# Performance work log

Hardware: AMD Instinct MI355X
Metric: run time of the kernel (lower is better)

Reference implementation:

```python
import jax, jax.numpy as jnp
import numpy as np

N = 50000      # nodes
E = 500000     # edges
IN_FEAT = 128
OUT_FEAT = 128
R = 200        # num_relations
NB = 16        # num_bases -> 8x8 blocks
SI = IN_FEAT // NB   # submat_in = 8
SO = OUT_FEAT // NB  # submat_out = 8


def setup_inputs() -> dict:
    key = jax.random.key(0)
    k1, k2, k3, k4, k5, k6, k7 = jax.random.split(key, 7)
    h = jax.random.normal(k1, (N, IN_FEAT), dtype=jnp.float32)
    norm = jax.random.uniform(k2, (N, 1), dtype=jnp.float32)
    weight = jax.random.normal(k3, (R, NB * SI * SO), dtype=jnp.float32) * 0.1
    loop_weight = jax.random.normal(k4, (IN_FEAT, OUT_FEAT), dtype=jnp.float32) * 0.1
    src = jax.random.randint(k5, (E,), 0, N, dtype=jnp.int32)
    dst = jax.random.randint(k6, (E,), 0, N, dtype=jnp.int32)
    etype = jax.random.randint(k7, (E,), 0, R, dtype=jnp.int32)
    return {"h": h, "norm": norm, "weight": weight, "loop_weight": loop_weight,
            "src": src, "dst": dst, "etype": etype}


def reference(h, norm, weight, loop_weight, src, dst, etype):
    # self-loop message: [N, out_feat]
    loop_message = h @ loop_weight
    # per-edge relation-weight gather: [E, NB, SI, SO]
    w_e = weight[etype].reshape(-1, NB, SI, SO)
    # src features as per-basis blocks: [E, NB, SI]
    x_e = h[src].reshape(-1, NB, SI)
    # block-diagonal bmm -> messages [E, out_feat]
    msg = jnp.einsum('ebi,ebio->ebo', x_e, w_e).reshape(-1, OUT_FEAT)
    # scatter-sum to destination nodes (fn.sum(msg -> h))
    agg = jax.ops.segment_sum(msg, dst, num_segments=N)
    # apply_func: multiply by per-node norm, then add self-loop and activation
    nodes = agg * norm
    nodes = nodes + loop_message
    return jax.nn.relu(nodes)
```

## Files before the change

### kernel.cpp

```cpp
#include <hip/hip_runtime.h>
#include <hip/hip_bf16.h>


#define IN_FEAT 128
#define OUT_FEAT 128
#define SCAN_CHUNK 512

using short8  = __attribute__((ext_vector_type(8))) short;
using float4v = __attribute__((ext_vector_type(4))) float;

__device__ inline float blo(unsigned u) { return __uint_as_float(u << 16); }
__device__ inline float bhi(unsigned u) { return __uint_as_float(u & 0xffff0000u); }
__device__ inline unsigned short f2bf(float f) {
  __hip_bfloat16 b = __float2bfloat16(f);
  return *reinterpret_cast<unsigned short*>(&b);
}

__device__ inline float dot2bf(unsigned x, unsigned w, float c) {
#if __has_builtin(__builtin_amdgcn_fdot2_f32_bf16)
  typedef __bf16 bf16x2 __attribute__((ext_vector_type(2)));
  return __builtin_amdgcn_fdot2_f32_bf16(__builtin_bit_cast(bf16x2, x),
                                         __builtin_bit_cast(bf16x2, w), c, false);
#else
  return c + blo(x) * blo(w) + bhi(x) * bhi(w);
#endif
}

__global__ __launch_bounds__(256) void k_prep(
    const float* __restrict__ w, unsigned short* __restrict__ w16,
    const float* __restrict__ h, uint4* __restrict__ h16p, int htotal8,
    const float* __restrict__ lw, unsigned short* __restrict__ lwT,
    const int* __restrict__ dst, int* __restrict__ cnt, int E,
    int bw, int bh, int blw) {
  __shared__ float srow[1024];
  const int bid = blockIdx.x;
  if (bid < bw) {
    const float* wr = w + ((size_t)bid << 10);
    ((float4*)srow)[threadIdx.x] = ((const float4*)wr)[threadIdx.x];
    __syncthreads();
    const int d0 = threadIdx.x * 4;
    unsigned short o4[4];
    #pragma unroll
    for (int k = 0; k < 4; ++k) {
      const int d = d0 + k;
      const int b = d >> 6;
      const int q = d & 63;
      const int opp = q >> 4;
      const int tt = q & 15;
      const int jj = tt >> 3;
      const int ii = tt & 7;
      o4[k] = f2bf(srow[b * 64 + ii * 8 + opp * 2 + jj]);
    }
    *(uint2*)(w16 + ((size_t)bid << 10) + d0) =
        make_uint2((unsigned)o4[0] | ((unsigned)o4[1] << 16),
                   (unsigned)o4[2] | ((unsigned)o4[3] << 16));
  } else if (bid < bw + bh) {
    const int t = (bid - bw) * 256 + threadIdx.x;
    if (t < htotal8) {
      const float4 a = ((const float4*)h)[2 * t];
      const float4 b = ((const float4*)h)[2 * t + 1];
      uint4 o;
      o.x = (unsigned)f2bf(a.x) | ((unsigned)f2bf(a.y) << 16);
      o.y = (unsigned)f2bf(a.z) | ((unsigned)f2bf(a.w) << 16);
      o.z = (unsigned)f2bf(b.x) | ((unsigned)f2bf(b.y) << 16);
      o.w = (unsigned)f2bf(b.z) | ((unsigned)f2bf(b.w) << 16);
      h16p[t] = o;
    }
  } else if (bid < bw + bh + blw) {
    const int idx = (bid - bw - bh) * 256 + threadIdx.x;
    if (idx < IN_FEAT * OUT_FEAT) {
      const int o = idx >> 7;
      const int k = idx & 127;
      lwT[idx] = f2bf(lw[k * 128 + o]);
    }
  } else {
    const int e0 = ((bid - bw - bh - blw) * 256 + threadIdx.x) * 4;
    if (e0 + 3 < E) {
      const int4 d4 = *(const int4*)(dst + e0);
      atomicAdd(&cnt[d4.x], 1);
      atomicAdd(&cnt[d4.y], 1);
      atomicAdd(&cnt[d4.z], 1);
      atomicAdd(&cnt[d4.w], 1);
    } else {
      for (int e = e0; e < E; ++e) atomicAdd(&cnt[dst[e]], 1);
    }
  }
}

__global__ __launch_bounds__(256) void k_offsets_sp(
    const int* __restrict__ cnt, int* __restrict__ pos, int N) {
  __shared__ int s[256];
  __shared__ int sbase;
  const int t = threadIdx.x;
  const int vb = blockIdx.x;
  {
    const int lim = vb * SCAN_CHUNK;
    int acc = 0;
    for (int i = t; i < lim; i += 256) acc += cnt[i];
    s[t] = acc;
    __syncthreads();
    for (int d = 128; d > 0; d >>= 1) {
      if (t < d) s[t] += s[t + d];
      __syncthreads();
    }
    if (t == 0) sbase = s[0];
    __syncthreads();
  }
  const int base = vb * SCAN_CHUNK;
  const int i0 = base + 2 * t;
  const int i1 = i0 + 1;
  const int c0 = (i0 < N) ? cnt[i0] : 0;
  const int c1 = (i1 < N) ? cnt[i1] : 0;
  const int pair = c0 + c1;
  s[t] = pair;
  __syncthreads();
  #pragma unroll
  for (int d = 1; d < 256; d <<= 1) {
    int v = (t >= d) ? s[t - d] : 0;
    __syncthreads();
    s[t] += v;
    __syncthreads();
  }
  const int ex = s[t] - pair + sbase;
  if (i0 < N) pos[i0] = ex;
  if (i1 < N) pos[i1] = ex + c0;
}

__global__ __launch_bounds__(256) void k_scatter(
    const int* __restrict__ src, const int* __restrict__ dst,
    const int* __restrict__ etype, int* __restrict__ pos,
    int2* __restrict__ srcet, int E) {
  const int e0 = (blockIdx.x * blockDim.x + threadIdx.x) * 4;
  if (e0 + 3 < E) {
    const int4 s4 = *(const int4*)(src + e0);
    const int4 d4 = *(const int4*)(dst + e0);
    const int4 t4 = *(const int4*)(etype + e0);
    int p;
    p = atomicAdd(&pos[d4.x], 1); srcet[p] = make_int2(s4.x, t4.x);
    p = atomicAdd(&pos[d4.y], 1); srcet[p] = make_int2(s4.y, t4.y);
    p = atomicAdd(&pos[d4.z], 1); srcet[p] = make_int2(s4.z, t4.z);
    p = atomicAdd(&pos[d4.w], 1); srcet[p] = make_int2(s4.w, t4.w);
  } else {
    for (int e = e0; e < E; ++e) {
      const int p = atomicAdd(&pos[dst[e]], 1);
      srcet[p] = make_int2(src[e], etype[e]);
    }
  }
}

__global__ __launch_bounds__(256) void agg_fused(
    const unsigned short* __restrict__ h16, const float* __restrict__ norm,
    const unsigned short* __restrict__ w16, const unsigned short* __restrict__ lwT,
    const int* __restrict__ pos, const int* __restrict__ cnt,
    const int2* __restrict__ srcet, float* __restrict__ out, int N) {
  __shared__ float lmsg[16][128];
  const int wid = threadIdx.x >> 6;
  const int lane = threadIdx.x & 63;
  const int node_base = blockIdx.x * 16;

  {
    const int m = lane & 15;
    const int kg = (lane >> 4) * 8;
    const int arow = min(node_base + m, N - 1);
    const unsigned short* ap = h16 + (size_t)arow * 128 + kg;
    const unsigned short* bp = lwT + (size_t)m * 128 + kg;
    const int nt0 = wid * 2, nt1 = wid * 2 + 1;

    float4v acc0 = (float4v){0.f, 0.f, 0.f, 0.f};
    float4v acc1 = (float4v){0.f, 0.f, 0.f, 0.f};
    #pragma unroll
    for (int kc = 0; kc < 4; ++kc) {
      const short8 a  = *(const short8*)(ap + kc * 32);
      const short8 b0 = *(const short8*)(bp + nt0 * 2048 + kc * 32);
      const short8 b1 = *(const short8*)(bp + nt1 * 2048 + kc * 32);
      acc0 = __builtin_amdgcn_mfma_f32_16x16x32_bf16(a, b0, acc0, 0, 0, 0);
      acc1 = __builtin_amdgcn_mfma_f32_16x16x32_bf16(a, b1, acc1, 0, 0, 0);
    }
    const int rrow = (lane >> 4) * 4;
    #pragma unroll
    for (int r = 0; r < 4; ++r) {
      lmsg[rrow + r][nt0 * 16 + m] = acc0[r];
      lmsg[rrow + r][nt1 * 16 + m] = acc1[r];
    }
  }
  __syncthreads();

  const int b = lane >> 2;
  const int opp = lane & 3;
  const int woff = b * 64 + opp * 16;
  const int o = b * 8 + opp * 2;

  for (int u = 0; u < 4; ++u) {
    const int node = node_base + wid * 4 + u;
    if (node >= N) continue;

    const int num = cnt[node];
    const int end = pos[node];
    const int begin = end - num;

    float a0 = 0.f, a1 = 0.f;

    for (int base = 0; base < num; base += 64) {
      const int cn = min(64, num - base);
      const int2 my = srcet[begin + base + min(lane, cn - 1)];
      for (int i4 = 0; i4 < cn; i4 += 4) {
        const int gl = min(i4 + (lane >> 4), cn - 1);
        const int sg = __shfl(my.x, gl);
        const uint4 xq =
            *(const uint4*)(h16 + ((size_t)sg << 7) + (lane & 15) * 8);
        const int nin = min(4, cn - i4);
        #pragma unroll 4
        for (int v = 0; v < nin; ++v) {
          const int r = __shfl(my.y, i4 + v);
          const int sl = v * 16 + b;
          uint4 xv;
          xv.x = __shfl(xq.x, sl);
          xv.y = __shfl(xq.y, sl);
          xv.z = __shfl(xq.z, sl);
          xv.w = __shfl(xq.w, sl);
          const unsigned short* wp = w16 + ((size_t)r << 10) + woff;
          const uint4 wa = *(const uint4*)(wp);
          const uint4 wb = *(const uint4*)(wp + 8);

          a0 = dot2bf(xv.x, wa.x, a0);
          a0 = dot2bf(xv.y, wa.y, a0);
          a0 = dot2bf(xv.z, wa.z, a0);
          a0 = dot2bf(xv.w, wa.w, a0);
          a1 = dot2bf(xv.x, wb.x, a1);
          a1 = dot2bf(xv.y, wb.y, a1);
          a1 = dot2bf(xv.z, wb.z, a1);
          a1 = dot2bf(xv.w, wb.w, a1);
        }
      }
    }

    const float nm = norm[node];
    const float2 prev = *(const float2*)&lmsg[wid * 4 + u][o];
    float2 res;
    res.x = fmaxf(prev.x + a0 * nm, 0.f);
    res.y = fmaxf(prev.y + a1 * nm, 0.f);
    *(float2*)(out + ((size_t)node << 7) + o) = res;
  }
}

__global__ __launch_bounds__(256) void k_hist(
    const int* __restrict__ dst, int* __restrict__ cnt, int E) {
  const int e = blockIdx.x * blockDim.x + threadIdx.x;
  if (e < E) atomicAdd(&cnt[dst[e]], 1);
}

__global__ __launch_bounds__(256) void selfloop_gemm(
    const float* __restrict__ h, const float* __restrict__ lw,
    float* __restrict__ out, int n) {
  __shared__ float slw[IN_FEAT * OUT_FEAT];
  __shared__ float sh[32 * IN_FEAT];

  {
    const float4* s4 = (const float4*)lw;
    float4* d4 = (float4*)slw;
    for (int i = threadIdx.x; i < IN_FEAT * OUT_FEAT / 4; i += 256) d4[i] = s4[i];
  }

  const int cg_ = threadIdx.x & 31;
  const int rg = threadIdx.x >> 5;

  for (int base = blockIdx.x * 32; base < n; base += gridDim.x * 32) {
    const int nrows = min(32, n - base);
    __syncthreads();
    {
      const float4* hs = (const float4*)(h + (size_t)base * IN_FEAT);
      float4* sd = (float4*)sh;
      const int cnt = nrows * (IN_FEAT / 4);
      for (int i = threadIdx.x; i < cnt; i += 256) sd[i] = hs[i];
    }
    __syncthreads();

    float4 acc[4];
    #pragma unroll
    for (int j = 0; j < 4; ++j) acc[j] = make_float4(0.f, 0.f, 0.f, 0.f);

    #pragma unroll 4
    for (int k = 0; k < IN_FEAT; ++k) {
      const float4 w = ((const float4*)slw)[k * 32 + cg_];
      #pragma unroll
      for (int j = 0; j < 4; ++j) {
        const float hv = sh[(rg + 8 * j) * IN_FEAT + k];
        acc[j].x += hv * w.x;
        acc[j].y += hv * w.y;
        acc[j].z += hv * w.z;
        acc[j].w += hv * w.w;
      }
    }

    #pragma unroll
    for (int j = 0; j < 4; ++j) {
      const int r = rg + 8 * j;
      if (r < nrows) {
        ((float4*)(out + (size_t)(base + r) * OUT_FEAT))[cg_] = acc[j];
      }
    }
  }
}

__global__ __launch_bounds__(256) void agg(
    const float* __restrict__ h, const float* __restrict__ norm,
    const float* __restrict__ weight, const int* __restrict__ pos,
    const int* __restrict__ cnt, const int2* __restrict__ srcet,
    float* __restrict__ out, int N) {
  const int node = (int)((blockIdx.x * blockDim.x + threadIdx.x) >> 6);
  const int lane = threadIdx.x & 63;
  if (node >= N) return;

  const int b = lane >> 2;
  const int op = (lane & 3) * 2;
  const int boff = b * 64 + op;

  const int num = cnt[node];
  const int end = pos[node];
  const int begin = end - num;

  float a0 = 0.f, a1 = 0.f;

  for (int base = 0; base < num; base += 64) {
    const int cn = min(64, num - base);
    const int2 my = srcet[begin + base + min(lane, cn - 1)];
    #pragma unroll 2
    for (int i = 0; i < cn; ++i) {
      const int s = __shfl(my.x, i);
      const int r = __shfl(my.y, i);
      const float* xp = h + ((size_t)s << 7) + b * 8;
      const float4 x0 = ((const float4*)xp)[0];
      const float4 x1 = ((const float4*)xp)[1];
      const float* wp = weight + ((size_t)r << 10) + boff;
      const float2 w0 = *(const float2*)(wp);
      const float2 w1 = *(const float2*)(wp + 8);
      const float2 w2 = *(const float2*)(wp + 16);
      const float2 w3 = *(const float2*)(wp + 24);
      const float2 w4 = *(const float2*)(wp + 32);
      const float2 w5 = *(const float2*)(wp + 40);
      const float2 w6 = *(const float2*)(wp + 48);
      const float2 w7 = *(const float2*)(wp + 56);
      a0 += x0.x * w0.x; a1 += x0.x * w0.y;
      a0 += x0.y * w1.x; a1 += x0.y * w1.y;
      a0 += x0.z * w2.x; a1 += x0.z * w2.y;
      a0 += x0.w * w3.x; a1 += x0.w * w3.y;
      a0 += x1.x * w4.x; a1 += x1.x * w4.y;
      a0 += x1.y * w5.x; a1 += x1.y * w5.y;
      a0 += x1.z * w6.x; a1 += x1.z * w6.y;
      a0 += x1.w * w7.x; a1 += x1.w * w7.y;
    }
  }

  const float nm = norm[node];
  const int o = b * 8 + op;
  float* outp = out + ((size_t)node << 7) + o;
  float2 prev = *(const float2*)outp;
  float2 res;
  res.x = fmaxf(prev.x + a0 * nm, 0.f);
  res.y = fmaxf(prev.y + a1 * nm, 0.f);
  *(float2*)outp = res;
}

__global__ __launch_bounds__(256) void edge_msg(
    const float* __restrict__ h, const float* __restrict__ norm,
    const float* __restrict__ weight, const int* __restrict__ src,
    const int* __restrict__ dst, const int* __restrict__ etype,
    float* out, int E) {
  const int wave = (int)((blockIdx.x * blockDim.x + threadIdx.x) >> 6);
  const int lane = threadIdx.x & 63;
  if (wave >= E) return;

  const int s = src[wave];
  const int d = dst[wave];
  const int r = etype[wave];
  const float nrm = norm[d];

  const int b = lane >> 2;
  const int op = (lane & 3) * 2;

  const float* xp = h + (size_t)s * IN_FEAT + b * 8;
  const float4 x0 = ((const float4*)xp)[0];
  const float4 x1 = ((const float4*)xp)[1];
  float x[8] = {x0.x, x0.y, x0.z, x0.w, x1.x, x1.y, x1.z, x1.w};

  const float* wp = weight + (size_t)r * 1024 + b * 64 + op;
  float a0 = 0.f, a1 = 0.f;
  #pragma unroll
  for (int i = 0; i < 8; ++i) {
    const float2 w = *(const float2*)(wp + i * 8);
    a0 += x[i] * w.x;
    a1 += x[i] * w.y;
  }

  const int o = b * 8 + op;
  float* outp = out + (size_t)d * OUT_FEAT + o;
  atomicAdd(outp, a0 * nrm);
  atomicAdd(outp + 1, a1 * nrm);
}

__global__ __launch_bounds__(256) void relu_k(float* __restrict__ out, int n4) {
  const int i = blockIdx.x * blockDim.x + threadIdx.x;
  if (i < n4) {
    float4 v = ((const float4*)out)[i];
    v.x = fmaxf(v.x, 0.f);
    v.y = fmaxf(v.y, 0.f);
    v.z = fmaxf(v.z, 0.f);
    v.w = fmaxf(v.w, 0.f);
    ((float4*)out)[i] = v;
  }
}

extern "C" void kernel_launch(void* const* d_in, const int* in_sizes, int n_in,
                              void* d_out, int out_size, void* d_ws, size_t ws_size,
                              hipStream_t stream) {
  const float* h    = (const float*)d_in[0];
  const float* norm = (const float*)d_in[1];
  const float* w    = (const float*)d_in[2];
  const float* lw   = (const float*)d_in[3];
  const int* src    = (const int*)d_in[4];
  const int* dst    = (const int*)d_in[5];
  const int* etype  = (const int*)d_in[6];
  float* out = (float*)d_out;

  const int N = in_sizes[1];
  const int E = in_sizes[4];
  const int R = in_sizes[2] / 1024;
  const int nblk = (N + SCAN_CHUNK - 1) / SCAN_CHUNK;

  const size_t nb_bsum = (size_t)((nblk < 128) ? 128 : nblk);
  const size_t off_cnt  = (size_t)E * 8;
  const size_t off_pos  = off_cnt + (size_t)N * 4;
  const size_t off_bsum = off_pos + (size_t)N * 4;
  size_t off_h16 = off_bsum + nb_bsum * 4;
  off_h16 = (off_h16 + 15) & ~(size_t)15;
  const size_t off_w16 = off_h16 + (size_t)N * IN_FEAT * 2;
  const size_t off_lwT = off_w16 + (size_t)R * 1024 * 2;
  const size_t need_full = off_lwT + (size_t)IN_FEAT * OUT_FEAT * 2;
  const size_t need_sort = off_bsum + nb_bsum * 4;

  if (ws_size >= need_full) {
    char* wsb = (char*)d_ws;
    int2* srcet = (int2*)wsb;
    int* cnt  = (int*)(wsb + off_cnt);
    int* pos  = (int*)(wsb + off_pos);
    unsigned short* h16 = (unsigned short*)(wsb + off_h16);
    unsigned short* w16 = (unsigned short*)(wsb + off_w16);
    unsigned short* lwT = (unsigned short*)(wsb + off_lwT);

    hipMemsetAsync(cnt, 0, (size_t)N * 4, stream);

    const int htotal8 = N * IN_FEAT / 8;
    const int bw  = R;
    const int bh  = (htotal8 + 255) / 256;
    const int blw = (IN_FEAT * OUT_FEAT + 255) / 256;
    const int bhist = (E + 1023) / 1024;
    k_prep<<<bw + bh + blw + bhist, 256, 0, stream>>>(
        w, w16, h, (uint4*)h16, htotal8, lw, lwT, dst, cnt, E, bw, bh, blw);

    k_offsets_sp<<<nblk, 256, 0, stream>>>(cnt, pos, N);
    k_scatter<<<(E + 1023) / 1024, 256, 0, stream>>>(src, dst, etype, pos,
                                                     srcet, E);

    agg_fused<<<(N + 15) / 16, 256, 0, stream>>>(h16, norm, w16, lwT, pos, cnt,
                                                 srcet, out, N);
  } else if (ws_size >= need_sort) {
    char* wsb = (char*)d_ws;
    int2* srcet = (int2*)wsb;
    int* cnt  = (int*)(wsb + off_cnt);
    int* pos  = (int*)(wsb + off_pos);

    selfloop_gemm<<<512, 256, 0, stream>>>(h, lw, out, N);
    hipMemsetAsync(cnt, 0, (size_t)N * 4, stream);
    k_hist<<<(E + 255) / 256, 256, 0, stream>>>(dst, cnt, E);
    k_offsets_sp<<<nblk, 256, 0, stream>>>(cnt, pos, N);
    k_scatter<<<(E + 1023) / 1024, 256, 0, stream>>>(src, dst, etype, pos,
                                                     srcet, E);
    agg<<<(N + 3) / 4, 256, 0, stream>>>(h, norm, w, pos, cnt, srcet, out, N);
  } else {
    selfloop_gemm<<<512, 256, 0, stream>>>(h, lw, out, N);
    edge_msg<<<(E + 3) / 4, 256, 0, stream>>>(h, norm, w, src, dst, etype, out, E);
    const int n4 = N * OUT_FEAT / 4;
    relu_k<<<(n4 + 255) / 256, 256, 0, stream>>>(out, n4);
  }
}
```

Measured before the change: 169.9 us.

## Move self-loop GEMM into prep kernel and simplify aggregation kernel

The self-loop GEMM (h @ loop_weight) moves out of the aggregation kernel into the k_prep launch. New blocks there convert loop_weight column slices to bf16 in shared memory and run MFMA on fp32 h converted on the fly, writing results straight to out. The aggregation kernel then maps one wavefront per node, reads the self-loop result back from out, and drops the shared-memory staging and block barrier. This overlaps the GEMM with the histogram and prep work and removes the lwT buffer, at the cost of an extra read and write pass over out. The weight-prep path now does scalar stores and sometimes falls back to global reads.

```diff
diff --git a/kernel.cpp b/kernel.cpp
--- a/kernel.cpp
+++ b/kernel.cpp
@@ -26,36 +26,53 @@
 #endif
 }
 
+__device__ inline short8 pack8(const float4 a, const float4 b) {
+  short8 r;
+  r[0] = (short)f2bf(a.x); r[1] = (short)f2bf(a.y);
+  r[2] = (short)f2bf(a.z); r[3] = (short)f2bf(a.w);
+  r[4] = (short)f2bf(b.x); r[5] = (short)f2bf(b.y);
+  r[6] = (short)f2bf(b.z); r[7] = (short)f2bf(b.w);
+  return r;
+}
+
 __global__ __launch_bounds__(256) void k_prep(
     const float* __restrict__ w, unsigned short* __restrict__ w16,
     const float* __restrict__ h, uint4* __restrict__ h16p, int htotal8,
-    const float* __restrict__ lw, unsigned short* __restrict__ lwT,
-    const int* __restrict__ dst, int* __restrict__ cnt, int E,
-    int bw, int bh, int blw) {
-  __shared__ float srow[1024];
+    const float* __restrict__ lw, const int* __restrict__ dst,
+    int* __restrict__ cnt, int E, float* __restrict__ out, int N,
+    int bw, int bh, int bg) {
+  __shared__ char smem[32 * 136 * 2];
   const int bid = blockIdx.x;
+  const int tid = threadIdx.x;
+
   if (bid < bw) {
+    float* srow = (float*)smem;
     const float* wr = w + ((size_t)bid << 10);
-    ((float4*)srow)[threadIdx.x] = ((const float4*)wr)[threadIdx.x];
-    __syncthreads();
-    const int d0 = threadIdx.x * 4;
-    unsigned short o4[4];
     #pragma unroll
-    for (int k = 0; k < 4; ++k) {
-      const int d = d0 + k;
-      const int b = d >> 6;
-      const int q = d & 63;
-      const int opp = q >> 4;
-      const int tt = q & 15;
-      const int jj = tt >> 3;
-      const int ii = tt & 7;
-      o4[k] = f2bf(srow[b * 64 + ii * 8 + opp * 2 + jj]);
-    }
-    *(uint2*)(w16 + ((size_t)bid << 10) + d0) =
-        make_uint2((unsigned)o4[0] | ((unsigned)o4[1] << 16),
-                   (unsigned)o4[2] | ((unsigned)o4[3] << 16));
+    for (int half = 0; half < 2; ++half) {
+      ((float2*)srow)[tid] = ((const float2*)(wr + half * 512))[tid];
+      __syncthreads();
+      #pragma unroll
+      for (int k = 0; k < 2; ++k) {
+        const int d = half * 512 + tid * 2 + k;
+        const int b = d >> 6;
+        const int q = d & 63;
+        const int opp = q >> 4;
+        const int tt = q & 15;
+        const int jj = tt >> 3;
+        const int ii = tt & 7;
+        const int srci = b * 64 + ii * 8 + opp * 2 + jj;
+        float v;
+        if (srci >= half * 512 && srci < half * 512 + 512)
+          v = srow[srci - half * 512];
+        else
+          v = wr[srci];
+        w16[((size_t)bid << 10) + d] = f2bf(v);
+      }
+      __syncthreads();
+    }
   } else if (bid < bw + bh) {
-    const int t = (bid - bw) * 256 + threadIdx.x;
+    const int t = (bid - bw) * 256 + tid;
     if (t < htotal8) {
       const float4 a = ((const float4*)h)[2 * t];
       const float4 b = ((const float4*)h)[2 * t + 1];
@@ -66,15 +83,63 @@
       o.w = (unsigned)f2bf(b.z) | ((unsigned)f2bf(b.w) << 16);
       h16p[t] = o;
     }
-  } else if (bid < bw + bh + blw) {
-    const int idx = (bid - bw - bh) * 256 + threadIdx.x;
-    if (idx < IN_FEAT * OUT_FEAT) {
-      const int o = idx >> 7;
-      const int k = idx & 127;
-      lwT[idx] = f2bf(lw[k * 128 + o]);
+  } else if (bid < bw + bh + bg) {
+    unsigned short* slw = (unsigned short*)smem;
+    const int g = bid - bw - bh;
+    const int vb = g >> 2;
+    const int cp = g & 3;
+
+    {
+      const float4* lw4 = (const float4*)lw;
+      for (int i = tid; i < 1024; i += 256) {
+        const int k = i >> 3;
+        const int cq = i & 7;
+        const float4 v = lw4[k * 32 + cp * 8 + cq];
+        const int cl = cq * 4;
+        slw[(cl + 0) * 136 + k] = f2bf(v.x);
+        slw[(cl + 1) * 136 + k] = f2bf(v.y);
+        slw[(cl + 2) * 136 + k] = f2bf(v.z);
+        slw[(cl + 3) * 136 + k] = f2bf(v.w);
+      }
+    }
+    __syncthreads();
+
+    const int wid = tid >> 6;
+    const int lane = tid & 63;
+    const int m = lane & 15;
+    const int kg = (lane >> 4) * 8;
+    const int row0 = vb * 64 + wid * 16;
+    if (row0 < N) {
+      const int arow = min(row0 + m, N - 1);
+      const float* hp = h + (size_t)arow * 128 + kg;
+      const unsigned short* bp0 = slw + (0 * 16 + m) * 136 + kg;
+      const unsigned short* bp1 = slw + (1 * 16 + m) * 136 + kg;
+
+      float4v acc0 = (float4v){0.f, 0.f, 0.f, 0.f};
+      float4v acc1 = (float4v){0.f, 0.f, 0.f, 0.f};
+      #pragma unroll
+      for (int kc = 0; kc < 4; ++kc) {
+        const float4 a0 = *(const float4*)(hp + kc * 32);
+        const float4 a1 = *(const float4*)(hp + kc * 32 + 4);
+        const short8 a = pack8(a0, a1);
+        const short8 b0 = *(const short8*)(bp0 + kc * 32);
+        const short8 b1 = *(const short8*)(bp1 + kc * 32);
+        acc0 = __builtin_amdgcn_mfma_f32_16x16x32_bf16(a, b0, acc0, 0, 0, 0);
+        acc1 = __builtin_amdgcn_mfma_f32_16x16x32_bf16(a, b1, acc1, 0, 0, 0);
+      }
+      const int crow = row0 + (lane >> 4) * 4;
+      const int col0 = cp * 32 + m;
+      #pragma unroll
+      for (int r = 0; r < 4; ++r) {
+        const int row = crow + r;
+        if (row < N) {
+          out[(size_t)row * 128 + col0] = acc0[r];
+          out[(size_t)row * 128 + col0 + 16] = acc1[r];
+        }
+      }
     }
   } else {
-    const int e0 = ((bid - bw - bh - blw) * 256 + threadIdx.x) * 4;
+    const int e0 = ((bid - bw - bh - bg) * 256 + tid) * 4;
     if (e0 + 3 < E) {
       const int4 d4 = *(const int4*)(dst + e0);
       atomicAdd(&cnt[d4.x], 1);
@@ -148,99 +213,68 @@
   }
 }
 
-__global__ __launch_bounds__(256) void agg_fused(
+__global__ __launch_bounds__(256) void agg_bf16(
     const unsigned short* __restrict__ h16, const float* __restrict__ norm,
-    const unsigned short* __restrict__ w16, const unsigned short* __restrict__ lwT,
-    const int* __restrict__ pos, const int* __restrict__ cnt,
-    const int2* __restrict__ srcet, float* __restrict__ out, int N) {
-  __shared__ float lmsg[16][128];
-  const int wid = threadIdx.x >> 6;
+    const unsigned short* __restrict__ w16, const int* __restrict__ pos,
+    const int* __restrict__ cnt, const int2* __restrict__ srcet,
+    float* __restrict__ out, int N) {
+  const int node = (int)((blockIdx.x * blockDim.x + threadIdx.x) >> 6);
   const int lane = threadIdx.x & 63;
-  const int node_base = blockIdx.x * 16;
-
-  {
-    const int m = lane & 15;
-    const int kg = (lane >> 4) * 8;
-    const int arow = min(node_base + m, N - 1);
-    const unsigned short* ap = h16 + (size_t)arow * 128 + kg;
-    const unsigned short* bp = lwT + (size_t)m * 128 + kg;
-    const int nt0 = wid * 2, nt1 = wid * 2 + 1;
-
-    float4v acc0 = (float4v){0.f, 0.f, 0.f, 0.f};
-    float4v acc1 = (float4v){0.f, 0.f, 0.f, 0.f};
-    #pragma unroll
-    for (int kc = 0; kc < 4; ++kc) {
-      const short8 a  = *(const short8*)(ap + kc * 32);
-      const short8 b0 = *(const short8*)(bp + nt0 * 2048 + kc * 32);
-      const short8 b1 = *(const short8*)(bp + nt1 * 2048 + kc * 32);
-      acc0 = __builtin_amdgcn_mfma_f32_16x16x32_bf16(a, b0, acc0, 0, 0, 0);
-      acc1 = __builtin_amdgcn_mfma_f32_16x16x32_bf16(a, b1, acc1, 0, 0, 0);
-    }
-    const int rrow = (lane >> 4) * 4;
-    #pragma unroll
-    for (int r = 0; r < 4; ++r) {
-      lmsg[rrow + r][nt0 * 16 + m] = acc0[r];
-      lmsg[rrow + r][nt1 * 16 + m] = acc1[r];
-    }
-  }
-  __syncthreads();
+  if (node >= N) return;
 
   const int b = lane >> 2;
   const int opp = lane & 3;
   const int woff = b * 64 + opp * 16;
   const int o = b * 8 + opp * 2;
 
-  for (int u = 0; u < 4; ++u) {
-    const int node = node_base + wid * 4 + u;
-    if (node >= N) continue;
-
-    const int num = cnt[node];
-    const int end = pos[node];
-    const int begin = end - num;
-
-    float a0 = 0.f, a1 = 0.f;
-
-    for (int base = 0; base < num; base += 64) {
-      const int cn = min(64, num - base);
-      const int2 my = srcet[begin + base + min(lane, cn - 1)];
-      for (int i4 = 0; i4 < cn; i4 += 4) {
-        const int gl = min(i4 + (lane >> 4), cn - 1);
-        const int sg = __shfl(my.x, gl);
-        const uint4 xq =
-            *(const uint4*)(h16 + ((size_t)sg << 7) + (lane & 15) * 8);
-        const int nin = min(4, cn - i4);
-        #pragma unroll 4
-        for (int v = 0; v < nin; ++v) {
-          const int r = __shfl(my.y, i4 + v);
-          const int sl = v * 16 + b;
-          uint4 xv;
-          xv.x = __shfl(xq.x, sl);
-          xv.y = __shfl(xq.y, sl);
-          xv.z = __shfl(xq.z, sl);
-          xv.w = __shfl(xq.w, sl);
-          const unsigned short* wp = w16 + ((size_t)r << 10) + woff;
-          const uint4 wa = *(const uint4*)(wp);
-          const uint4 wb = *(const uint4*)(wp + 8);
-
-          a0 = dot2bf(xv.x, wa.x, a0);
-          a0 = dot2bf(xv.y, wa.y, a0);
-          a0 = dot2bf(xv.z, wa.z, a0);
-          a0 = dot2bf(xv.w, wa.w, a0);
-          a1 = dot2bf(xv.x, wb.x, a1);
-          a1 = dot2bf(xv.y, wb.y, a1);
-          a1 = dot2bf(xv.z, wb.z, a1);
-          a1 = dot2bf(xv.w, wb.w, a1);
-        }
-      }
-    }
-
-    const float nm = norm[node];
-    const float2 prev = *(const float2*)&lmsg[wid * 4 + u][o];
-    float2 res;
-    res.x = fmaxf(prev.x + a0 * nm, 0.f);
-    res.y = fmaxf(prev.y + a1 * nm, 0.f);
-    *(float2*)(out + ((size_t)node << 7) + o) = res;
-  }
+  const int num = cnt[node];
+  const int end = pos[node];
+  const int begin = end - num;
+
+  float* outp = out + ((size_t)node << 7) + o;
+  const float2 prev = *(const float2*)outp;
+  const float nm = norm[node];
+
+  float a0 = 0.f, a1 = 0.f;
+
+  for (int base = 0; base < num; base += 64) {
+    const int cn = min(64, num - base);
+    const int2 my = srcet[begin + base + min(lane, cn - 1)];
+    for (int i4 = 0; i4 < cn; i4 += 4) {
+      const int gl = min(i4 + (lane >> 4), cn - 1);
+      const int sg = __shfl(my.x, gl);
+      const uint4 xq =
+          *(const uint4*)(h16 + ((size_t)sg << 7) + (lane & 15) * 8);
+      const int nin = min(4, cn - i4);
+      #pragma unroll 4
+      for (int u = 0; u < nin; ++u) {
+        const int r = __shfl(my.y, i4 + u);
+        const int sl = u * 16 + b;
+        uint4 xv;
+        xv.x = __shfl(xq.x, sl);
+        xv.y = __shfl(xq.y, sl);
+        xv.z = __shfl(xq.z, sl);
+        xv.w = __shfl(xq.w, sl);
+        const unsigned short* wp = w16 + ((size_t)r << 10) + woff;
+        const uint4 wa = *(const uint4*)(wp);
+        const uint4 wb = *(const uint4*)(wp + 8);
+
+        a0 = dot2bf(xv.x, wa.x, a0);
+        a0 = dot2bf(xv.y, wa.y, a0);
+        a0 = dot2bf(xv.z, wa.z, a0);
+        a0 = dot2bf(xv.w, wa.w, a0);
+        a1 = dot2bf(xv.x, wb.x, a1);
+        a1 = dot2bf(xv.y, wb.y, a1);
+        a1 = dot2bf(xv.z, wb.z, a1);
+        a1 = dot2bf(xv.w, wb.w, a1);
+      }
+    }
+  }
+
+  float2 res;
+  res.x = fmaxf(prev.x + a0 * nm, 0.f);
+  res.y = fmaxf(prev.y + a1 * nm, 0.f);
+  *(float2*)outp = res;
 }
 
 __global__ __launch_bounds__(256) void k_hist(
@@ -434,8 +468,7 @@
   size_t off_h16 = off_bsum + nb_bsum * 4;
   off_h16 = (off_h16 + 15) & ~(size_t)15;
   const size_t off_w16 = off_h16 + (size_t)N * IN_FEAT * 2;
-  const size_t off_lwT = off_w16 + (size_t)R * 1024 * 2;
-  const size_t need_full = off_lwT + (size_t)IN_FEAT * OUT_FEAT * 2;
+  const size_t need_full = off_w16 + (size_t)R * 1024 * 2;
   const size_t need_sort = off_bsum + nb_bsum * 4;
 
   if (ws_size >= need_full) {
@@ -445,24 +478,23 @@
     int* pos  = (int*)(wsb + off_pos);
     unsigned short* h16 = (unsigned short*)(wsb + off_h16);
     unsigned short* w16 = (unsigned short*)(wsb + off_w16);
-    unsigned short* lwT = (unsigned short*)(wsb + off_lwT);
 
     hipMemsetAsync(cnt, 0, (size_t)N * 4, stream);
 
     const int htotal8 = N * IN_FEAT / 8;
     const int bw  = R;
     const int bh  = (htotal8 + 255) / 256;
-    const int blw = (IN_FEAT * OUT_FEAT + 255) / 256;
+    const int bg  = ((N + 63) / 64) * 4;
     const int bhist = (E + 1023) / 1024;
-    k_prep<<<bw + bh + blw + bhist, 256, 0, stream>>>(
-        w, w16, h, (uint4*)h16, htotal8, lw, lwT, dst, cnt, E, bw, bh, blw);
+    k_prep<<<bw + bh + bg + bhist, 256, 0, stream>>>(
+        w, w16, h, (uint4*)h16, htotal8, lw, dst, cnt, E, out, N, bw, bh, bg);
 
     k_offsets_sp<<<nblk, 256, 0, stream>>>(cnt, pos, N);
     k_scatter<<<(E + 1023) / 1024, 256, 0, stream>>>(src, dst, etype, pos,
                                                      srcet, E);
 
-    agg_fused<<<(N + 15) / 16, 256, 0, stream>>>(h16, norm, w16, lwT, pos, cnt,
-                                                 srcet, out, N);
+    agg_bf16<<<(N + 3) / 4, 256, 0, stream>>>(h16, norm, w16, pos, cnt, srcet,
+                                              out, N);
   } else if (ws_size >= need_sort) {
     char* wsb = (char*)d_ws;
     int2* srcet = (int2*)wsb;
```

New measurement: 163.8 us. 3.6% less time.
